# Optimization experiments

Hardware: AMD Instinct MI355X
Metric: run time of the kernel (lower is better)

## Reference

```python
import jax, jax.numpy as jnp
import numpy as np

N, D, D_QK, D_V = 8192, 1024, 128, 128

def setup_inputs() -> dict:
    key = jax.random.key(0)
    k1, k2, k3, k4 = jax.random.split(key, 4)
    s = 1.0 / np.sqrt(D)
    return {
        "x": jax.random.normal(k1, (N, D), dtype=jnp.float32),
        "Wq": jax.random.normal(k2, (D_QK, D), dtype=jnp.float32) * s,
        "Wk": jax.random.normal(k3, (D_QK, D), dtype=jnp.float32) * s,
        "Wv": jax.random.normal(k4, (D_V, D), dtype=jnp.float32) * s,
    }

def reference(x, Wq, Wk, Wv):
    # NOTE: original code MULTIPLIES by sqrt(D_qk) (dq_sqrt_inv = np.sqrt(D_qk)).
    scale = jnp.sqrt(jnp.asarray(D_QK, dtype=x.dtype))
    q = x @ Wq.T            # [N, D_qk]
    k = x @ Wk.T            # [N, D_qk]
    v = x @ Wv.T            # [N, D_v]
    scores = scale * (q @ k.T)          # [N, N]
    attn = jax.nn.softmax(scores, axis=-1)
    return attn @ v          # [N, D_v]
```

## Files before the change

### kernel.cpp

```cpp
#include <hip/hip_runtime.h>
#include <hip/hip_bf16.h>
#include <math.h>

#define N_TOK 8192
#define D_IN  1024
#define D_H   128
#define SPLIT 8

typedef __bf16 bf16;
typedef __attribute__((ext_vector_type(4))) __bf16 bf16x4;
typedef __attribute__((ext_vector_type(8))) __bf16 bf16x8;
typedef __attribute__((ext_vector_type(4))) float floatx4;

#define MFMA16(a, b, c) __builtin_amdgcn_mfma_f32_16x16x32_bf16((a), (b), (c), 0, 0, 0)

__device__ __forceinline__ size_t vtf_idx(int n, int d) {
    return ((size_t)((n >> 6) * 8 + (d >> 4)) << 10)
         + (((n >> 3) & 7) << 7) + ((d & 15) << 3) + (n & 7);
}
__device__ __forceinline__ size_t khf_idx(int n, int d) {
    return ((size_t)(((n >> 6) * 4 + (d >> 5)) * 4 + ((n >> 4) & 3)) << 9)
         + (((d >> 3) & 3) << 7) + ((n & 15) << 3) + (d & 7);
}

#define PJ_BM 64
#define PJ_BK 64
#define PJ_LS 72

__global__ __launch_bounds__(256)
void qkv_kernel(const float* __restrict__ x,
                const float* __restrict__ Wq,
                const float* __restrict__ Wk,
                const float* __restrict__ Wv,
                bf16* __restrict__ q_hi, bf16* __restrict__ q_lo,
                bf16* __restrict__ khf, bf16* __restrict__ klf,
                bf16* __restrict__ vtf)
{
    const float* W = (blockIdx.y == 0) ? Wq : (blockIdx.y == 1) ? Wk : Wv;

    __shared__ bf16 ah_s[PJ_BM][PJ_LS];
    __shared__ bf16 al_s[PJ_BM][PJ_LS];
    __shared__ bf16 bh_s[D_H][PJ_LS];
    __shared__ bf16 bl_s[D_H][PJ_LS];

    const int t    = threadIdx.x;
    const int lane = t & 63;
    const int wid  = t >> 6;
    const int wr   = wid >> 1;
    const int wc   = wid & 1;
    const int lid  = lane & 15;
    const int quad = lane >> 4;
    const int m0   = blockIdx.x * PJ_BM;

    floatx4 acc[2][4];
    #pragma unroll
    for (int s2 = 0; s2 < 2; ++s2)
        #pragma unroll
        for (int ct = 0; ct < 4; ++ct)
            #pragma unroll
            for (int r = 0; r < 4; ++r) acc[s2][ct][r] = 0.f;

    for (int k0 = 0; k0 < D_IN; k0 += PJ_BK) {
        __syncthreads();
        #pragma unroll
        for (int i = 0; i < 4; ++i) {
            int f  = t + i * 256;
            int r  = f >> 4;
            int c4 = (f & 15) << 2;
            float4 xv = *(const float4*)&x[(size_t)(m0 + r) * D_IN + k0 + c4];
            bf16x4 h, l;
            float vv[4] = { xv.x, xv.y, xv.z, xv.w };
            #pragma unroll
            for (int j = 0; j < 4; ++j) {
                bf16 hh = (bf16)vv[j];
                h[j] = hh;
                l[j] = (bf16)(vv[j] - (float)hh);
            }
            *(bf16x4*)&ah_s[r][c4] = h;
            *(bf16x4*)&al_s[r][c4] = l;
        }
        #pragma unroll
        for (int i = 0; i < 8; ++i) {
            int f  = t + i * 256;
            int r  = f >> 4;
            int c4 = (f & 15) << 2;
            float4 wv = *(const float4*)&W[(size_t)r * D_IN + k0 + c4];
            bf16x4 h, l;
            float vv[4] = { wv.x, wv.y, wv.z, wv.w };
            #pragma unroll
            for (int j = 0; j < 4; ++j) {
                bf16 hh = (bf16)vv[j];
                h[j] = hh;
                l[j] = (bf16)(vv[j] - (float)hh);
            }
            *(bf16x4*)&bh_s[r][c4] = h;
            *(bf16x4*)&bl_s[r][c4] = l;
        }
        __syncthreads();

        #pragma unroll
        for (int kc = 0; kc < 2; ++kc) {
            bf16x8 ah[2], al[2], bh[4], bl[4];
            #pragma unroll
            for (int s2 = 0; s2 < 2; ++s2) {
                ah[s2] = *(const bf16x8*)&ah_s[wr * 32 + s2 * 16 + lid][kc * 32 + quad * 8];
                al[s2] = *(const bf16x8*)&al_s[wr * 32 + s2 * 16 + lid][kc * 32 + quad * 8];
            }
            #pragma unroll
            for (int ct = 0; ct < 4; ++ct) {
                bh[ct] = *(const bf16x8*)&bh_s[wc * 64 + ct * 16 + lid][kc * 32 + quad * 8];
                bl[ct] = *(const bf16x8*)&bl_s[wc * 64 + ct * 16 + lid][kc * 32 + quad * 8];
            }
            #pragma unroll
            for (int s2 = 0; s2 < 2; ++s2)
                #pragma unroll
                for (int ct = 0; ct < 4; ++ct) {
                    acc[s2][ct] = MFMA16(ah[s2], bh[ct], acc[s2][ct]);
                    acc[s2][ct] = MFMA16(al[s2], bh[ct], acc[s2][ct]);
                    acc[s2][ct] = MFMA16(ah[s2], bl[ct], acc[s2][ct]);
                }
        }
    }

    if (blockIdx.y == 0) {
        const float sc = 11.313708498984760390f;
        #pragma unroll
        for (int s2 = 0; s2 < 2; ++s2)
            #pragma unroll
            for (int ct = 0; ct < 4; ++ct)
                #pragma unroll
                for (int r = 0; r < 4; ++r) {
                    int row = m0 + wr * 32 + s2 * 16 + quad * 4 + r;
                    int col = wc * 64 + ct * 16 + lid;
                    float a = acc[s2][ct][r] * sc;
                    bf16 h = (bf16)a;
                    q_hi[(size_t)row * D_H + col] = h;
                    q_lo[(size_t)row * D_H + col] = (bf16)(a - (float)h);
                }
    } else if (blockIdx.y == 1) {
        #pragma unroll
        for (int s2 = 0; s2 < 2; ++s2)
            #pragma unroll
            for (int ct = 0; ct < 4; ++ct)
                #pragma unroll
                for (int r = 0; r < 4; ++r) {
                    int n = m0 + wr * 32 + s2 * 16 + quad * 4 + r;
                    int d = wc * 64 + ct * 16 + lid;
                    float a = acc[s2][ct][r];
                    bf16 h = (bf16)a;
                    size_t idx = khf_idx(n, d);
                    khf[idx] = h;
                    klf[idx] = (bf16)(a - (float)h);
                }
    } else {
        #pragma unroll
        for (int s2 = 0; s2 < 2; ++s2)
            #pragma unroll
            for (int ct = 0; ct < 4; ++ct)
                #pragma unroll
                for (int r = 0; r < 4; ++r) {
                    int n = m0 + wr * 32 + s2 * 16 + quad * 4 + r;
                    int d = wc * 64 + ct * 16 + lid;
                    vtf[vtf_idx(n, d)] = (bf16)acc[s2][ct][r];
                }
    }
}

#define BQ   128
#define BKEY 64

__global__ __launch_bounds__(256, 2)
void flash_kernel(const bf16* __restrict__ qh, const bf16* __restrict__ ql,
                  const bf16* __restrict__ khf, const bf16* __restrict__ klf,
                  const bf16* __restrict__ vtf,
                  bf16*  __restrict__ opart,
                  float* __restrict__ mpart,
                  float* __restrict__ lpart)
{
    __shared__ bf16 kh_s[BKEY * D_H];
    __shared__ bf16 kl_s[BKEY * D_H];
    __shared__ bf16 p_s[4 * 2048];

    const int t     = threadIdx.x;
    const int lane  = t & 63;
    const int wid   = t >> 6;
    const int lid   = lane & 15;
    const int quad  = lane >> 4;
    const int q0    = blockIdx.x * BQ;
    const int strip = wid * 32;
    const int sp    = blockIdx.y;
    const int tile0 = sp * (N_TOK / BKEY / SPLIT);
    const int tile1 = tile0 + (N_TOK / BKEY / SPLIT);

    bf16x8 a_hi[2][4], a_lo[2][4];
    #pragma unroll
    for (int m = 0; m < 2; ++m) {
        const size_t rowb = (size_t)(q0 + strip + m * 16 + lid) * D_H + quad * 8;
        #pragma unroll
        for (int kc = 0; kc < 4; ++kc) {
            a_hi[m][kc] = *(const bf16x8*)(qh + rowb + kc * 32);
            a_lo[m][kc] = *(const bf16x8*)(ql + rowb + kc * 32);
        }
    }

    bf16x8 vones;
    #pragma unroll
    for (int j = 0; j < 8; ++j) vones[j] = (bf16)1.0f;

    float m_run[2][4];
    #pragma unroll
    for (int m = 0; m < 2; ++m)
        #pragma unroll
        for (int r = 0; r < 4; ++r) m_run[m][r] = -INFINITY;
    floatx4 l_acc[2];
    #pragma unroll
    for (int m = 0; m < 2; ++m)
        #pragma unroll
        for (int r = 0; r < 4; ++r) l_acc[m][r] = 0.f;
    floatx4 o_acc[2][8];
    #pragma unroll
    for (int m = 0; m < 2; ++m)
        #pragma unroll
        for (int ct = 0; ct < 8; ++ct)
            #pragma unroll
            for (int r = 0; r < 4; ++r) o_acc[m][ct][r] = 0.f;

    auto stage = [&](int tile) {
        const bf16* gh = khf + ((size_t)tile << 13) + (wid << 11) + (lane << 3);
        const bf16* gl = klf + ((size_t)tile << 13) + (wid << 11) + (lane << 3);
        bf16* lh = kh_s + (wid << 11);
        bf16* ll = kl_s + (wid << 11);
        #pragma unroll
        for (int i = 0; i < 4; ++i) {
            __builtin_amdgcn_global_load_lds(
                (const __attribute__((address_space(1))) void*)(gh + i * 512),
                (__attribute__((address_space(3))) void*)(lh + i * 512), 16, 0, 0);
            __builtin_amdgcn_global_load_lds(
                (const __attribute__((address_space(1))) void*)(gl + i * 512),
                (__attribute__((address_space(3))) void*)(ll + i * 512), 16, 0, 0);
        }
    };

    stage(tile0);

    for (int tt = tile0; tt < tile1; ++tt) {
        __syncthreads();

        floatx4 s[2][4];
        #pragma unroll
        for (int m = 0; m < 2; ++m)
            #pragma unroll
            for (int ct = 0; ct < 4; ++ct)
                #pragma unroll
                for (int r = 0; r < 4; ++r) s[m][ct][r] = 0.f;

        #pragma unroll
        for (int kc = 0; kc < 4; ++kc)
            #pragma unroll
            for (int ct = 0; ct < 4; ++ct) {
                const int fo = ((kc * 4 + ct) << 9) + (lane << 3);
                bf16x8 bh = *(const bf16x8*)&kh_s[fo];
                bf16x8 bl = *(const bf16x8*)&kl_s[fo];
                #pragma unroll
                for (int m = 0; m < 2; ++m) {
                    s[m][ct] = MFMA16(a_hi[m][kc], bh, s[m][ct]);
                    s[m][ct] = MFMA16(a_lo[m][kc], bh, s[m][ct]);
                    s[m][ct] = MFMA16(a_hi[m][kc], bl, s[m][ct]);
                }
            }

        __syncthreads();
        if (tt + 1 < tile1) stage(tt + 1);

        const bf16* vb = vtf + (((size_t)tt * 8) << 10) + (lane << 3);
        bf16x8 bv0[8];
        #pragma unroll
        for (int ct = 0; ct < 8; ++ct)
            bv0[ct] = *(const bf16x8*)(vb + ((size_t)ct << 10));

        float alpha[2][4];
        #pragma unroll
        for (int m = 0; m < 2; ++m)
            #pragma unroll
            for (int r = 0; r < 4; ++r) {
                float mx = fmaxf(fmaxf(s[m][0][r], s[m][1][r]),
                                 fmaxf(s[m][2][r], s[m][3][r]));
                #pragma unroll
                for (int off = 1; off < 16; off <<= 1)
                    mx = fmaxf(mx, __shfl_xor(mx, off, 64));
                float mn = fmaxf(m_run[m][r], mx);
                alpha[m][r] = __expf(m_run[m][r] - mn);
                m_run[m][r] = mn;
                #pragma unroll
                for (int ct = 0; ct < 4; ++ct) {
                    float p = __expf(s[m][ct][r] - mn);
                    int fl = (((m * 2 + (ct >> 1)) << 6)
                              + (((ct & 1) * 2 + (lid >> 3)) << 4)
                              + quad * 4 + r) * 8 + (lid & 7);
                    p_s[(wid << 11) + fl] = (bf16)p;
                }
            }

        bool need = false;
        #pragma unroll
        for (int m = 0; m < 2; ++m)
            #pragma unroll
            for (int r = 0; r < 4; ++r) need |= (alpha[m][r] != 1.0f);
        if (__any(need)) {
            #pragma unroll
            for (int m = 0; m < 2; ++m) {
                #pragma unroll
                for (int r = 0; r < 4; ++r) l_acc[m][r] *= alpha[m][r];
                #pragma unroll
                for (int ct = 0; ct < 8; ++ct)
                    #pragma unroll
                    for (int r = 0; r < 4; ++r)
                        o_acc[m][ct][r] *= alpha[m][r];
            }
        }

        {
            bf16x8 ap0[2];
            #pragma unroll
            for (int m = 0; m < 2; ++m)
                ap0[m] = *(const bf16x8*)&p_s[(wid << 11) + (((m * 2 + 0) << 6) << 3)
                                              + (lane << 3)];
            #pragma unroll
            for (int m = 0; m < 2; ++m)
                l_acc[m] = MFMA16(ap0[m], vones, l_acc[m]);
            #pragma unroll
            for (int ct = 0; ct < 8; ++ct)
                #pragma unroll
                for (int m = 0; m < 2; ++m)
                    o_acc[m][ct] = MFMA16(ap0[m], bv0[ct], o_acc[m][ct]);

            bf16x8 bv1[8];
            #pragma unroll
            for (int ct = 0; ct < 8; ++ct)
                bv1[ct] = *(const bf16x8*)(vb + ((size_t)ct << 10) + 512);
            bf16x8 ap1[2];
            #pragma unroll
            for (int m = 0; m < 2; ++m)
                ap1[m] = *(const bf16x8*)&p_s[(wid << 11) + (((m * 2 + 1) << 6) << 3)
                                              + (lane << 3)];
            #pragma unroll
            for (int m = 0; m < 2; ++m)
                l_acc[m] = MFMA16(ap1[m], vones, l_acc[m]);
            #pragma unroll
            for (int ct = 0; ct < 8; ++ct)
                #pragma unroll
                for (int m = 0; m < 2; ++m)
                    o_acc[m][ct] = MFMA16(ap1[m], bv1[ct], o_acc[m][ct]);
        }
    }

    bf16* op = opart + (size_t)sp * N_TOK * D_H;
    #pragma unroll
    for (int m = 0; m < 2; ++m)
        #pragma unroll
        for (int ct = 0; ct < 8; ++ct)
            #pragma unroll
            for (int r = 0; r < 4; ++r)
                op[(size_t)(q0 + strip + m * 16 + quad * 4 + r) * D_H
                   + ct * 16 + lid] = (bf16)o_acc[m][ct][r];
    if (lid == 0) {
        #pragma unroll
        for (int m = 0; m < 2; ++m)
            #pragma unroll
            for (int r = 0; r < 4; ++r) {
                int row = q0 + strip + m * 16 + quad * 4 + r;
                mpart[(size_t)sp * N_TOK + row] = m_run[m][r];
                lpart[(size_t)sp * N_TOK + row] = l_acc[m][r];
            }
    }
}

__global__ __launch_bounds__(256)
void combine_kernel(const bf16* __restrict__ opart,
                    const float* __restrict__ mpart,
                    const float* __restrict__ lpart,
                    float* __restrict__ out)
{
    const int t   = threadIdx.x;
    const int row = blockIdx.x * 16 + (t >> 4);
    const int c0  = (t & 15) * 8;

    float ms[SPLIT], ls[SPLIT];
    float mstar = -INFINITY;
    #pragma unroll
    for (int s = 0; s < SPLIT; ++s) {
        ms[s] = mpart[(size_t)s * N_TOK + row];
        ls[s] = lpart[(size_t)s * N_TOK + row];
        mstar = fmaxf(mstar, ms[s]);
    }
    float acc[8] = {};
    float L = 0.f;
    #pragma unroll
    for (int s = 0; s < SPLIT; ++s) {
        float w = __expf(ms[s] - mstar);
        L += w * ls[s];
        bf16x8 o = *(const bf16x8*)&opart[((size_t)s * N_TOK + row) * D_H + c0];
        #pragma unroll
        for (int j = 0; j < 8; ++j)
            acc[j] += w * (float)o[j];
    }
    float inv = 1.f / L;
    float* dst = &out[(size_t)row * D_H + c0];
    *(float4*)(dst + 0) = make_float4(acc[0] * inv, acc[1] * inv,
                                      acc[2] * inv, acc[3] * inv);
    *(float4*)(dst + 4) = make_float4(acc[4] * inv, acc[5] * inv,
                                      acc[6] * inv, acc[7] * inv);
}

extern "C" void kernel_launch(void* const* d_in, const int* in_sizes, int n_in,
                              void* d_out, int out_size, void* d_ws, size_t ws_size,
                              hipStream_t stream) {
    const float* x  = (const float*)d_in[0];
    const float* Wq = (const float*)d_in[1];
    const float* Wk = (const float*)d_in[2];
    const float* Wv = (const float*)d_in[3];
    float* out = (float*)d_out;

    bf16* wsb = (bf16*)d_ws;
    const size_t SZ = (size_t)N_TOK * D_H;
    bf16* qh  = wsb;
    bf16* ql  = wsb + SZ;
    bf16* khf = wsb + 2 * SZ;
    bf16* klf = wsb + 3 * SZ;
    bf16* vtf = wsb + 4 * SZ;
    bf16* opart = wsb + 5 * SZ;
    float* mpart = (float*)(wsb + (5 + SPLIT) * SZ);
    float* lpart = mpart + (size_t)SPLIT * N_TOK;

    qkv_kernel<<<dim3(N_TOK / PJ_BM, 3), 256, 0, stream>>>(x, Wq, Wk, Wv,
                                                           qh, ql, khf, klf, vtf);
    flash_kernel<<<dim3(N_TOK / BQ, SPLIT), 256, 0, stream>>>(qh, ql, khf, klf, vtf,
                                                              opart, mpart, lpart);
    combine_kernel<<<dim3(N_TOK / 16), 256, 0, stream>>>(opart, mpart, lpart, out);
}
```

Before: 196.8 us.

## Pre-split x and W into MFMA-fragment bf16 layout; raise flash split and occupancy

Adds a separate conversion kernel that splits x and the weights once into hi/lo bf16 pairs, stored in an MFMA-fragment-ordered layout. The projection kernel then loads fragments straight from global memory, with no shared-memory staging, barriers or repeated per-block conversion of W. The flash kernel's key split rises from 8 to 12, with uneven tile boundaries handled by rounding, and launch bounds ask for 3 blocks per CU. In exchange it adds an extra kernel launch, writes and rereads about 32MB of converted x, and uses a larger workspace plus more combine work.

```diff
diff --git a/kernel.cpp b/kernel.cpp
--- a/kernel.cpp
+++ b/kernel.cpp
@@ -5,7 +5,7 @@
 #define N_TOK 8192
 #define D_IN  1024
 #define D_H   128
-#define SPLIT 8
+#define SPLIT 12
 
 typedef __bf16 bf16;
 typedef __attribute__((ext_vector_type(4))) __bf16 bf16x4;
@@ -23,26 +23,60 @@
          + (((d >> 3) & 3) << 7) + ((n & 15) << 3) + (d & 7);
 }
 
-#define PJ_BM 64
-#define PJ_BK 64
-#define PJ_LS 72
+#define X_OCT (N_TOK * D_IN / 8)
+#define W_OCT (3 * D_H * D_IN / 8)
 
 __global__ __launch_bounds__(256)
-void qkv_kernel(const float* __restrict__ x,
-                const float* __restrict__ Wq,
-                const float* __restrict__ Wk,
-                const float* __restrict__ Wv,
+void convert_kernel(const float* __restrict__ x,
+                    const float* __restrict__ Wq,
+                    const float* __restrict__ Wk,
+                    const float* __restrict__ Wv,
+                    bf16* __restrict__ xhf, bf16* __restrict__ xlf,
+                    bf16* __restrict__ whf, bf16* __restrict__ wlf)
+{
+    const int gid = blockIdx.x * 256 + threadIdx.x;
+    const float* src;
+    bf16 *dh, *dl;
+    size_t doff;
+    if (gid < X_OCT) {
+        int lane = gid & 63, fc = gid >> 6;
+        int kc = fc & 31, mt = fc >> 5;
+        int n  = mt * 16 + (lane & 15);
+        int k0 = kc * 32 + ((lane >> 4) << 3);
+        src = x + (size_t)n * D_IN + k0;
+        dh = xhf; dl = xlf; doff = (size_t)gid << 3;
+    } else {
+        int w = gid - X_OCT;
+        int y = w >> 14, r = w & 16383;
+        int lane = r & 63, fc = r >> 6;
+        int kc = fc & 31, ct = fc >> 5;
+        int col = ct * 16 + (lane & 15);
+        int k0  = kc * 32 + ((lane >> 4) << 3);
+        const float* W = (y == 0) ? Wq : (y == 1) ? Wk : Wv;
+        src = W + (size_t)col * D_IN + k0;
+        dh = whf; dl = wlf; doff = (size_t)w << 3;
+    }
+    float4 a = *(const float4*)src;
+    float4 b = *(const float4*)(src + 4);
+    float vv[8] = { a.x, a.y, a.z, a.w, b.x, b.y, b.z, b.w };
+    bf16x8 h, l;
+    #pragma unroll
+    for (int j = 0; j < 8; ++j) {
+        bf16 hh = (bf16)vv[j];
+        h[j] = hh;
+        l[j] = (bf16)(vv[j] - (float)hh);
+    }
+    *(bf16x8*)(dh + doff) = h;
+    *(bf16x8*)(dl + doff) = l;
+}
+
+__global__ __launch_bounds__(256)
+void qkv_kernel(const bf16* __restrict__ xhf, const bf16* __restrict__ xlf,
+                const bf16* __restrict__ whf, const bf16* __restrict__ wlf,
                 bf16* __restrict__ q_hi, bf16* __restrict__ q_lo,
                 bf16* __restrict__ khf, bf16* __restrict__ klf,
                 bf16* __restrict__ vtf)
 {
-    const float* W = (blockIdx.y == 0) ? Wq : (blockIdx.y == 1) ? Wk : Wv;
-
-    __shared__ bf16 ah_s[PJ_BM][PJ_LS];
-    __shared__ bf16 al_s[PJ_BM][PJ_LS];
-    __shared__ bf16 bh_s[D_H][PJ_LS];
-    __shared__ bf16 bl_s[D_H][PJ_LS];
-
     const int t    = threadIdx.x;
     const int lane = t & 63;
     const int wid  = t >> 6;
@@ -50,75 +84,39 @@
     const int wc   = wid & 1;
     const int lid  = lane & 15;
     const int quad = lane >> 4;
-    const int m0   = blockIdx.x * PJ_BM;
+    const int m0   = blockIdx.x * 64;
+    const int mt0  = (m0 >> 4) + wr * 2;
+    const bf16* wh = whf + ((size_t)blockIdx.y << 17);
+    const bf16* wl = wlf + ((size_t)blockIdx.y << 17);
 
     floatx4 acc[2][4];
     #pragma unroll
-    for (int s2 = 0; s2 < 2; ++s2)
+    for (int m = 0; m < 2; ++m)
         #pragma unroll
         for (int ct = 0; ct < 4; ++ct)
             #pragma unroll
-            for (int r = 0; r < 4; ++r) acc[s2][ct][r] = 0.f;
-
-    for (int k0 = 0; k0 < D_IN; k0 += PJ_BK) {
-        __syncthreads();
-        #pragma unroll
-        for (int i = 0; i < 4; ++i) {
-            int f  = t + i * 256;
-            int r  = f >> 4;
-            int c4 = (f & 15) << 2;
-            float4 xv = *(const float4*)&x[(size_t)(m0 + r) * D_IN + k0 + c4];
-            bf16x4 h, l;
-            float vv[4] = { xv.x, xv.y, xv.z, xv.w };
-            #pragma unroll
-            for (int j = 0; j < 4; ++j) {
-                bf16 hh = (bf16)vv[j];
-                h[j] = hh;
-                l[j] = (bf16)(vv[j] - (float)hh);
+            for (int r = 0; r < 4; ++r) acc[m][ct][r] = 0.f;
+
+    #pragma unroll 4
+    for (int kc = 0; kc < 32; ++kc) {
+        bf16x8 ah[2], al[2];
+        #pragma unroll
+        for (int m = 0; m < 2; ++m) {
+            const size_t xb = ((size_t)((mt0 + m) * 32 + kc) << 9) + (lane << 3);
+            ah[m] = *(const bf16x8*)(xhf + xb);
+            al[m] = *(const bf16x8*)(xlf + xb);
+        }
+        #pragma unroll
+        for (int ct = 0; ct < 4; ++ct) {
+            const size_t wb = ((size_t)((wc * 4 + ct) * 32 + kc) << 9) + (lane << 3);
+            bf16x8 bh = *(const bf16x8*)(wh + wb);
+            bf16x8 bl = *(const bf16x8*)(wl + wb);
+            #pragma unroll
+            for (int m = 0; m < 2; ++m) {
+                acc[m][ct] = MFMA16(ah[m], bh, acc[m][ct]);
+                acc[m][ct] = MFMA16(al[m], bh, acc[m][ct]);
+                acc[m][ct] = MFMA16(ah[m], bl, acc[m][ct]);
             }
-            *(bf16x4*)&ah_s[r][c4] = h;
-            *(bf16x4*)&al_s[r][c4] = l;
-        }
-        #pragma unroll
-        for (int i = 0; i < 8; ++i) {
-            int f  = t + i * 256;
-            int r  = f >> 4;
-            int c4 = (f & 15) << 2;
-            float4 wv = *(const float4*)&W[(size_t)r * D_IN + k0 + c4];
-            bf16x4 h, l;
-            float vv[4] = { wv.x, wv.y, wv.z, wv.w };
-            #pragma unroll
-            for (int j = 0; j < 4; ++j) {
-                bf16 hh = (bf16)vv[j];
-                h[j] = hh;
-                l[j] = (bf16)(vv[j] - (float)hh);
-            }
-            *(bf16x4*)&bh_s[r][c4] = h;
-            *(bf16x4*)&bl_s[r][c4] = l;
-        }
-        __syncthreads();
-
-        #pragma unroll
-        for (int kc = 0; kc < 2; ++kc) {
-            bf16x8 ah[2], al[2], bh[4], bl[4];
-            #pragma unroll
-            for (int s2 = 0; s2 < 2; ++s2) {
-                ah[s2] = *(const bf16x8*)&ah_s[wr * 32 + s2 * 16 + lid][kc * 32 + quad * 8];
-                al[s2] = *(const bf16x8*)&al_s[wr * 32 + s2 * 16 + lid][kc * 32 + quad * 8];
-            }
-            #pragma unroll
-            for (int ct = 0; ct < 4; ++ct) {
-                bh[ct] = *(const bf16x8*)&bh_s[wc * 64 + ct * 16 + lid][kc * 32 + quad * 8];
-                bl[ct] = *(const bf16x8*)&bl_s[wc * 64 + ct * 16 + lid][kc * 32 + quad * 8];
-            }
-            #pragma unroll
-            for (int s2 = 0; s2 < 2; ++s2)
-                #pragma unroll
-                for (int ct = 0; ct < 4; ++ct) {
-                    acc[s2][ct] = MFMA16(ah[s2], bh[ct], acc[s2][ct]);
-                    acc[s2][ct] = MFMA16(al[s2], bh[ct], acc[s2][ct]);
-                    acc[s2][ct] = MFMA16(ah[s2], bl[ct], acc[s2][ct]);
-                }
         }
     }
 
@@ -169,7 +167,7 @@
 #define BQ   128
 #define BKEY 64
 
-__global__ __launch_bounds__(256, 2)
+__global__ __launch_bounds__(256, 3)
 void flash_kernel(const bf16* __restrict__ qh, const bf16* __restrict__ ql,
                   const bf16* __restrict__ khf, const bf16* __restrict__ klf,
                   const bf16* __restrict__ vtf,
@@ -189,8 +187,8 @@
     const int q0    = blockIdx.x * BQ;
     const int strip = wid * 32;
     const int sp    = blockIdx.y;
-    const int tile0 = sp * (N_TOK / BKEY / SPLIT);
-    const int tile1 = tile0 + (N_TOK / BKEY / SPLIT);
+    const int tile0 = (sp * (N_TOK / BKEY)) / SPLIT;
+    const int tile1 = ((sp + 1) * (N_TOK / BKEY)) / SPLIT;
 
     bf16x8 a_hi[2][4], a_lo[2][4];
     #pragma unroll
@@ -423,18 +421,24 @@
 
     bf16* wsb = (bf16*)d_ws;
     const size_t SZ = (size_t)N_TOK * D_H;
-    bf16* qh  = wsb;
-    bf16* ql  = wsb + SZ;
-    bf16* khf = wsb + 2 * SZ;
-    bf16* klf = wsb + 3 * SZ;
-    bf16* vtf = wsb + 4 * SZ;
-    bf16* opart = wsb + 5 * SZ;
-    float* mpart = (float*)(wsb + (5 + SPLIT) * SZ);
+    bf16* xhf = wsb;
+    bf16* xlf = xhf + (size_t)X_OCT * 8;
+    bf16* whf = xlf + (size_t)X_OCT * 8;
+    bf16* wlf = whf + (size_t)W_OCT * 8;
+    bf16* qh  = wlf + (size_t)W_OCT * 8;
+    bf16* ql  = qh + SZ;
+    bf16* khf = ql + SZ;
+    bf16* klf = khf + SZ;
+    bf16* vtf = klf + SZ;
+    bf16* opart = vtf + SZ;
+    float* mpart = (float*)(opart + (size_t)SPLIT * SZ);
     float* lpart = mpart + (size_t)SPLIT * N_TOK;
 
-    qkv_kernel<<<dim3(N_TOK / PJ_BM, 3), 256, 0, stream>>>(x, Wq, Wk, Wv,
-                                                           qh, ql, khf, klf, vtf);
-    flash_kernel<<<dim3(N_TOK / BQ, SPLIT), 256, 0, stream>>>(qh, ql, khf, klf, vtf,
-                                                              opart, mpart, lpart);
+    convert_kernel<<<dim3((X_OCT + W_OCT) / 256), 256, 0, stream>>>(
+        x, Wq, Wk, Wv, xhf, xlf, whf, wlf);
+    qkv_kernel<<<dim3(N_TOK / 64, 3), 256, 0, stream>>>(
+        xhf, xlf, whf, wlf, qh, ql, khf, klf, vtf);
+    flash_kernel<<<dim3(N_TOK / BQ, SPLIT), 256, 0, stream>>>(
+        qh, ql, khf, klf, vtf, opart, mpart, lpart);
     combine_kernel<<<dim3(N_TOK / 16), 256, 0, stream>>>(opart, mpart, lpart, out);
 }
```

After: 372.5 us. +89.3%, slower.
